# Optimization experiments

Measured on AMD Instinct MI355X. Metric: run time of the kernel, lower is better.

The kernel has to match this reference:

```python
import jax, jax.numpy as jnp
import numpy as np

B, L, E, A, H = 1024, 200, 128, 128, 4

def setup_inputs() -> dict:
    key = jax.random.key(0)
    k1, k2, k3, k4, k5, k6 = jax.random.split(key, 6)
    inp = jax.random.normal(k1, (B, L, E), dtype=jnp.float32)
    mask = jax.random.randint(k2, (B, L), 0, 2).astype(bool)
    # guarantee at least one valid position per row (realistic: histories are non-empty)
    mask = mask.at[:, 0].set(True)
    pos_enc = jax.random.normal(k3, (1, L, E), dtype=jnp.float32)
    W1 = jax.random.normal(k4, (E, A), dtype=jnp.float32) / np.sqrt(E)
    W2 = jax.random.normal(k5, (A, H), dtype=jnp.float32) / np.sqrt(A)
    W_out = jax.random.normal(k6, (H * E, E), dtype=jnp.float32) / np.sqrt(H * E)
    return {"input": inp, "mask": mask, "pos_enc": pos_enc, "W1": W1, "W2": W2, "W_out": W_out}

def reference(input, mask, pos_enc, W1, W2, W_out):
    fm = mask.astype(input.dtype)[..., None]          # [B, L, 1]
    x = input * fm                                     # zero out padded positions
    xp = x + pos_enc                                   # broadcast [1, L, E]
    hidden = jnp.tanh(xp @ W1)                         # [B, L, A]
    att = hidden @ W2                                  # [B, L, H]
    att = jnp.swapaxes(att, 1, 2)                      # [B, H, L]
    neg = jnp.asarray(-(2.0 ** 32) + 1.0, dtype=att.dtype)
    att = jnp.where(mask[:, None, :], att, neg)
    att = jax.nn.softmax(att, axis=-1)                 # [B, H, L]
    pooled = jnp.einsum('bhl,ble->bhe', att, x)        # [B, H, E]
    flat = pooled.reshape(pooled.shape[0], -1)         # [B, H*E]
    return flat @ W_out                                # [B, E]
```

## Files before the change

kernel.cpp:

```cpp
#include <hip/hip_runtime.h>
#include <cfloat>

#define Bn 1024
#define Ln 200
#define En 128
#define An 128
#define Hn 4

#define WS_POSW1   0
#define WS_W1FRAG  106496
#define WS_ATTPOOL 139264
#define SLOT       1664
#define WS_WOUTT   1843200
#define WS_NEEDED  1974272

using f32x4  = __attribute__((ext_vector_type(4))) float;
using bf16x8 = __attribute__((ext_vector_type(8))) short;

__device__ __forceinline__ unsigned short f2bf(float f){
    unsigned u = __builtin_bit_cast(unsigned, f);
    u = (u + 0x7FFFu + ((u >> 16) & 1u)) >> 16;
    return (unsigned short)u;
}
__device__ __forceinline__ float bf2f(unsigned short s){
    unsigned u = ((unsigned)s) << 16;
    return __builtin_bit_cast(float, u);
}
__device__ __forceinline__ float tanh_cheap(float x){
    float e = __expf(2.f * x);
    float r = __builtin_amdgcn_rcpf(e + 1.f);
    return fmaf(-2.f, r, 1.f);
}
__device__ __forceinline__ float tanh_fast(float x){
    x = fminf(fmaxf(x, -12.f), 12.f);
    float e = __expf(2.f * x);
    return 1.f - 2.f / (e + 1.f);
}
__device__ __forceinline__ unsigned cvt_pk_bf16(float lo, float hi){
    unsigned r;
    asm("v_cvt_pk_bf16_f32 %0, %1, %2" : "=v"(r) : "v"(lo), "v"(hi));
    return r;
}
__device__ __forceinline__ int swz(int row, int k){
    return row * 128 + ((((k >> 3) ^ (row & 15)) << 3) | (k & 7));
}

__global__ __launch_bounds__(256) void sap_prep(
    const float* __restrict__ pos, const float* __restrict__ W1,
    const float* __restrict__ Wout, void* __restrict__ ws)
{
    const int t = threadIdx.x, blk = blockIdx.x;
    if (blk < 104){
        float* posW1 = (float*)((char*)ws + WS_POSW1);
        int l = blk * 2 + (t >> 7), a = t & 127;
        float acc = 0.f;
        if (l < Ln){
            #pragma unroll 4
            for (int k = 0; k < 128; ++k)
                acc += pos[l * En + k] * W1[k * An + a];
        }
        posW1[l * An + a] = acc;
    } else if (blk < 106){
        unsigned short* w1f = (unsigned short*)((char*)ws + WS_W1FRAG);
        int s = (blk - 104) * 256 + t;
        int lane = s & 63;
        int A = s >> 6;
        int c = lane & 15, q = lane >> 4;
        #pragma unroll
        for (int ks = 0; ks < 4; ++ks){
            unsigned short v[8];
            #pragma unroll
            for (int j = 0; j < 8; ++j)
                v[j] = f2bf(W1[(ks * 32 + q * 8 + j) * An + A * 16 + c]);
            *(bf16x8*)&w1f[(s * 4 + ks) * 8] = *(bf16x8*)v;
        }
    } else {
        unsigned short* wt = (unsigned short*)((char*)ws + WS_WOUTT);
        int flat = ((blk - 106) * 256 + t) * 4;
        int e = flat >> 9, k = flat & 511;
        unsigned short v[4];
        #pragma unroll
        for (int i = 0; i < 4; ++i)
            v[i] = f2bf(Wout[(size_t)(k + i) * En + e]);
        *(uint2*)&wt[flat] = *(uint2*)v;
    }
}

__global__ __launch_bounds__(512, 4) void sap_att7(
    const float* __restrict__ inp, const void* __restrict__ maskp,
    const float* __restrict__ W2, void* __restrict__ ws)
{
    __shared__ unsigned short s_x[64 * 128];
    __shared__ float s_part[8][4][64];
    __shared__ float s_att4[208 * 4];
    __shared__ float s_scr[16][512];
    __shared__ float s_mask[256];

    const int t = threadIdx.x, lane = t & 63, w = t >> 6;
    const int c = lane & 15, q = lane >> 4;
    const int b = blockIdx.x;

    const unsigned short* w1f   = (const unsigned short*)((char*)ws + WS_W1FRAG);
    const float*          posW1 = (const float*)((char*)ws + WS_POSW1);
    unsigned short*       slot  = (unsigned short*)((char*)ws + WS_ATTPOOL + (size_t)b * SLOT);

    bf16x8 af[4];
    #pragma unroll
    for (int ks = 0; ks < 4; ++ks)
        af[ks] = *(const bf16x8*)&w1f[((w * 64 + lane) * 4 + ks) * 8];
    float4 w2a[4];
    #pragma unroll
    for (int v = 0; v < 4; ++v)
        w2a[v] = *(const float4*)&W2[(w * 16 + q * 4 + v) * Hn];

    {
        unsigned word = ((const unsigned*)maskp)[lane];
        unsigned long long bi  = __ballot(word > 1u);
        unsigned long long bfm = __ballot(word != 0u && word != 0x3F800000u);
        int flag = (bi == 0ull) ? 0 : ((bfm == 0ull) ? 2 : 1);
        if (t < 256){
            float m = 0.f;
            if (t < Ln){
                int mv;
                if (flag == 0)      mv = ((const int*)maskp)[b * Ln + t] != 0;
                else if (flag == 1) mv = ((const unsigned char*)maskp)[b * Ln + t] != 0;
                else                mv = ((const float*)maskp)[b * Ln + t] != 0.f;
                m = mv ? 1.f : 0.f;
            }
            s_mask[t] = m;
        }
    }

    for (int cch = 0; cch < 4; ++cch){
        const int NT = (cch < 3) ? 4 : 1;

        {
            const float4* in4 = (const float4*)(inp + (size_t)b * (Ln * En) + cch * 64 * En);
            #define PUTV(vi, idx) { int ll = (idx) >> 5, kk = ((idx) & 31) * 4;            \
                uint2 val = make_uint2(cvt_pk_bf16(vi.x, vi.y), cvt_pk_bf16(vi.z, vi.w));  \
                *(uint2*)&s_x[swz(ll, kk)] = val; }
            if (cch < 3){
                float4 u0 = in4[t], u1 = in4[t + 512], u2 = in4[t + 1024], u3 = in4[t + 1536];
                PUTV(u0, t) PUTV(u1, t + 512) PUTV(u2, t + 1024) PUTV(u3, t + 1536)
            } else {
                uint2 val = make_uint2(0u, 0u);
                if (t < 256){
                    float4 u0 = in4[t];
                    val = make_uint2(cvt_pk_bf16(u0.x, u0.y), cvt_pk_bf16(u0.z, u0.w));
                }
                int ll = t >> 5, kk = (t & 31) * 4;
                *(uint2*)&s_x[swz(ll, kk)] = val;
            }
            #undef PUTV
        }
        __syncthreads();

        for (int lt = 0; lt < NT; ++lt){
            int brow = lt * 16 + c;
            bf16x8 bfr[4];
            #pragma unroll
            for (int ks = 0; ks < 4; ++ks){
                int g = (ks * 4 + q) ^ c;
                bfr[ks] = *(bf16x8*)&s_x[brow * 128 + (g << 3)];
            }
            f32x4 acc = *(const f32x4*)&posW1[(size_t)(cch * 64 + brow) * An + w * 16 + q * 4];
            #pragma unroll
            for (int ks = 0; ks < 4; ++ks)
                acc = __builtin_amdgcn_mfma_f32_16x16x32_bf16(af[ks], bfr[ks], acc, 0, 0, 0);
            float contrib[4] = {0.f, 0.f, 0.f, 0.f};
            #pragma unroll
            for (int v = 0; v < 4; ++v){
                float hv = tanh_cheap(acc[v]);
                contrib[0] += hv * w2a[v].x;
                contrib[1] += hv * w2a[v].y;
                contrib[2] += hv * w2a[v].z;
                contrib[3] += hv * w2a[v].w;
            }
            #pragma unroll
            for (int h = 0; h < 4; ++h){
                contrib[h] += __shfl_xor(contrib[h], 16, 64);
                contrib[h] += __shfl_xor(contrib[h], 32, 64);
            }
            s_part[w][q][lt * 16 + c] = contrib[q];
        }
        __syncthreads();

        if (t < 256){
            int h = t >> 6, l = t & 63, gl = cch * 64 + l;
            if (gl < Ln){
                float a = 0.f;
                #pragma unroll
                for (int w2 = 0; w2 < 8; ++w2) a += s_part[w2][h][l];
                s_att4[gl * 4 + h] = (s_mask[gl] > 0.5f) ? a : -1.0e30f;
            }
        }
    }
    __syncthreads();

    if (t < 256){
        const int h = t >> 6, sl = t & 63;
        float v[4]; float mx = -FLT_MAX;
        #pragma unroll
        for (int i = 0; i < 4; ++i){
            int l = sl + i * 64;
            v[i] = (l < Ln) ? s_att4[l * 4 + h] : -3.0e38f;
            mx = fmaxf(mx, v[i]);
        }
        for (int s = 32; s; s >>= 1) mx = fmaxf(mx, __shfl_xor(mx, s, 64));
        float e[4]; float sum = 0.f;
        #pragma unroll
        for (int i = 0; i < 4; ++i){
            int l = sl + i * 64;
            e[i] = (l < Ln) ? __expf(v[i] - mx) : 0.f;
            sum += e[i];
        }
        for (int s = 32; s; s >>= 1) sum += __shfl_xor(sum, s, 64);
        float inv = 1.f / sum;
        #pragma unroll
        for (int i = 0; i < 4; ++i){
            int l = sl + i * 64;
            if (l < Ln) s_att4[l * 4 + h] = e[i] * inv;
        }
    }
    __syncthreads();

    {
        const int eg = t & 31, r = t >> 5;
        const float* xin = inp + (size_t)b * (Ln * En);
        f32x4 a0 = {0.f,0.f,0.f,0.f}, a1 = a0, a2 = a0, a3 = a0;
        for (int i = 0; i < 13; ++i){
            int l = i * 16 + r;
            if (l < Ln){
                f32x4 xv = *(const f32x4*)&xin[l * En + eg * 4];
                f32x4 w4 = *(const f32x4*)&s_att4[l * 4];
                a0 += xv * w4[0];
                a1 += xv * w4[1];
                a2 += xv * w4[2];
                a3 += xv * w4[3];
            }
        }
        *(f32x4*)&s_scr[r][0 * 128 + eg * 4] = a0;
        *(f32x4*)&s_scr[r][1 * 128 + eg * 4] = a1;
        *(f32x4*)&s_scr[r][2 * 128 + eg * 4] = a2;
        *(f32x4*)&s_scr[r][3 * 128 + eg * 4] = a3;
    }
    __syncthreads();

    {
        float sum = 0.f;
        #pragma unroll
        for (int r2 = 0; r2 < 16; ++r2) sum += s_scr[r2][t];
        slot[t] = f2bf(sum);
    }
}

__global__ __launch_bounds__(256) void sap_out(
    const void* __restrict__ ws, float* __restrict__ out)
{
    const unsigned short* wt = (const unsigned short*)((const char*)ws + WS_WOUTT);
    const int t = threadIdx.x, lane = t & 63, w = t >> 6;
    const int c = lane & 15, q = lane >> 4;
    const int b0 = blockIdx.x * 16;
    const int e0 = (blockIdx.y * 4 + w) * 16;

    const unsigned short* pslot =
        (const unsigned short*)((const char*)ws + WS_ATTPOOL + (size_t)(b0 + c) * SLOT);

    f32x4 acc = {0.f, 0.f, 0.f, 0.f};
    #pragma unroll 4
    for (int ks = 0; ks < 16; ++ks){
        bf16x8 afr = *(const bf16x8*)&pslot[ks * 32 + q * 8];
        bf16x8 bfr = *(const bf16x8*)&wt[(e0 + c) * 512 + ks * 32 + q * 8];
        acc = __builtin_amdgcn_mfma_f32_16x16x32_bf16(afr, bfr, acc, 0, 0, 0);
    }
    #pragma unroll
    for (int v = 0; v < 4; ++v)
        out[(size_t)(b0 + q * 4 + v) * En + e0 + c] = acc[v];
}

__global__ __launch_bounds__(512, 4) void sap_fused_v2(
    const float* __restrict__ inp, const void* __restrict__ maskp,
    const float* __restrict__ pos, const float* __restrict__ W1,
    const float* __restrict__ W2, const float* __restrict__ Wout,
    float* __restrict__ out)
{
#define LP 208
    __shared__ unsigned short s_xp [LP * 128];
    __shared__ float s_att [4 * LP];
    __shared__ float s_mask[LP];
    __shared__ float s_pool[512];
    __shared__ float s_red [512];
    __shared__ int   s_flag;

    const int t = threadIdx.x;
    const int b = blockIdx.x;
    const int lane = t & 63, w = t >> 6;
    const int c = lane & 15, q = lane >> 4;

    if (t == 0){
        const unsigned* mw = (const unsigned*)maskp;
        int fi = 1, ff = 1;
        for (int i = 0; i < 64; ++i){
            unsigned word = mw[i];
            if (word > 1u) fi = 0;
            if (word != 0u && word != 0x3F800000u) ff = 0;
        }
        s_flag = fi ? 0 : (ff ? 2 : 1);
    }
    bf16x8 af[4];
    {
        const int arow = w * 16 + c;
        #pragma unroll
        for (int ks = 0; ks < 4; ++ks)
            #pragma unroll
            for (int j = 0; j < 8; ++j)
                af[ks][j] = (short)f2bf(W1[(ks * 32 + q * 8 + j) * An + arow]);
    }
    float w2a[4][4];
    #pragma unroll
    for (int v = 0; v < 4; ++v){
        float4 wv = *(const float4*)&W2[(w * 16 + q * 4 + v) * Hn];
        w2a[v][0] = wv.x; w2a[v][1] = wv.y; w2a[v][2] = wv.z; w2a[v][3] = wv.w;
    }
    __syncthreads();
    const int flag = s_flag;
    for (int l = t; l < LP; l += 512){
        float m = 0.f;
        if (l < Ln){
            int mv;
            if (flag == 0)      mv = ((const int*)maskp)[b * Ln + l] != 0;
            else if (flag == 1) mv = ((const unsigned char*)maskp)[b * Ln + l] != 0;
            else                mv = ((const float*)maskp)[b * Ln + l] != 0.f;
            m = mv ? 1.f : 0.f;
        }
        s_mask[l] = m;
    }
    for (int i = t; i < 4 * LP; i += 512) s_att[i] = 0.f;
    __syncthreads();
    {
        const float4* in4 = (const float4*)(inp + (size_t)b * (Ln * En));
        const float4* p4  = (const float4*)pos;
        #pragma unroll
        for (int it = 0; it < 13; ++it){
            int idx = it * 512 + t;
            int l = idx >> 5;
            int k = (idx & 31) * 4;
            uint2 val;
            if (idx < 6400){
                float m = s_mask[l];
                float4 a = in4[idx];
                float4 p = p4[idx];
                val = make_uint2((unsigned)f2bf(a.x*m+p.x) | ((unsigned)f2bf(a.y*m+p.y) << 16),
                                 (unsigned)f2bf(a.z*m+p.z) | ((unsigned)f2bf(a.w*m+p.w) << 16));
            } else val = make_uint2(0u, 0u);
            *(uint2*)&s_xp[swz(l, k)] = val;
        }
    }
    __syncthreads();
    for (int lt = 0; lt < 13; ++lt){
        int brow = lt * 16 + c;
        bf16x8 bfr[4];
        #pragma unroll
        for (int ks = 0; ks < 4; ++ks){
            int g = (ks * 4 + q) ^ c;
            bfr[ks] = *(bf16x8*)&s_xp[brow * 128 + (g << 3)];
        }
        f32x4 acc = {0.f, 0.f, 0.f, 0.f};
        #pragma unroll
        for (int ks = 0; ks < 4; ++ks)
            acc = __builtin_amdgcn_mfma_f32_16x16x32_bf16(af[ks], bfr[ks], acc, 0, 0, 0);
        float hv[4];
        #pragma unroll
        for (int v = 0; v < 4; ++v) hv[v] = tanh_fast(acc[v]);
        #pragma unroll
        for (int h = 0; h < 4; ++h){
            float contrib = hv[0]*w2a[0][h] + hv[1]*w2a[1][h] + hv[2]*w2a[2][h] + hv[3]*w2a[3][h];
            contrib += __shfl_xor(contrib, 16, 64);
            contrib += __shfl_xor(contrib, 32, 64);
            if (lane < 16) atomicAdd(&s_att[h * LP + lt * 16 + lane], contrib);
        }
    }
    __syncthreads();
    if (t < 256){
        const int sl = t & 63, h = t >> 6;
        float v[4]; bool ok[4]; float mx = -FLT_MAX;
        #pragma unroll
        for (int i = 0; i < 4; ++i){
            int l = sl + i * 64;
            ok[i] = (l < Ln) && (s_mask[l] > 0.5f);
            v[i]  = ok[i] ? s_att[h * LP + l] : -FLT_MAX;
            mx = fmaxf(mx, v[i]);
        }
        for (int s = 32; s; s >>= 1) mx = fmaxf(mx, __shfl_xor(mx, s, 64));
        float e[4]; float sum = 0.f;
        #pragma unroll
        for (int i = 0; i < 4; ++i){ e[i] = ok[i] ? __expf(v[i]-mx) : 0.f; sum += e[i]; }
        for (int s = 32; s; s >>= 1) sum += __shfl_xor(sum, s, 64);
        float inv = 1.f / sum;
        #pragma unroll
        for (int i = 0; i < 4; ++i){ int l = sl + i*64; if (l < LP) s_att[h*LP+l] = e[i]*inv; }
    }
    __syncthreads();
    {
        int h = t >> 7, e = t & 127;
        float acc = 0.f;
        #pragma unroll 4
        for (int l = 0; l < Ln; ++l){
            float xv = bf2f(s_xp[swz(l, e)]) - pos[l * En + e];
            acc += s_att[h * LP + l] * xv;
        }
        s_pool[h * En + e] = acc;
    }
    __syncthreads();
    {
        int qt = t >> 7, e = t & 127;
        float acc = 0.f;
        const float* wo = Wout + (size_t)(qt * 128) * En + e;
        #pragma unroll 4
        for (int i = 0; i < 128; ++i)
            acc += s_pool[qt * 128 + i] * wo[(size_t)i * En];
        s_red[t] = acc;
    }
    __syncthreads();
    if (t < 128)
        out[(size_t)b * En + t] = s_red[t] + s_red[t + 128] + s_red[t + 256] + s_red[t + 384];
#undef LP
}

extern "C" void kernel_launch(void* const* d_in, const int* in_sizes, int n_in,
                              void* d_out, int out_size, void* d_ws, size_t ws_size,
                              hipStream_t stream)
{
    const float* inp  = (const float*)d_in[0];
    const void*  mask = d_in[1];
    const float* pos  = (const float*)d_in[2];
    const float* W1   = (const float*)d_in[3];
    const float* W2   = (const float*)d_in[4];
    const float* Wout = (const float*)d_in[5];
    float* out = (float*)d_out;

    if (ws_size >= WS_NEEDED){
        sap_prep<<<170, 256, 0, stream>>>(pos, W1, Wout, d_ws);
        sap_att7<<<Bn, 512, 0, stream>>>(inp, mask, W2, d_ws);
        sap_out<<<dim3(64, 2), 256, 0, stream>>>(d_ws, out);
    } else {
        sap_fused_v2<<<Bn, 512, 0, stream>>>(inp, mask, pos, W1, W2, Wout, out);
    }
}
```

Measured before the change: 64.60 us.

## Keep all input chunks in LDS as bf16 and pool from shared memory

```diff
diff --git a/kernel.cpp b/kernel.cpp
--- a/kernel.cpp
+++ b/kernel.cpp
@@ -86,14 +86,13 @@
     }
 }
 
-__global__ __launch_bounds__(512, 4) void sap_att7(
+__global__ __launch_bounds__(512, 4) void sap_att9(
     const float* __restrict__ inp, const void* __restrict__ maskp,
     const float* __restrict__ W2, void* __restrict__ ws)
 {
-    __shared__ unsigned short s_x[64 * 128];
+    __shared__ unsigned short s_x4[4][64 * 128];
     __shared__ float s_part[8][4][64];
     __shared__ float s_att4[208 * 4];
-    __shared__ float s_scr[16][512];
     __shared__ float s_mask[256];
 
     const int t = threadIdx.x, lane = t & 63, w = t >> 6;
@@ -133,6 +132,7 @@
 
     for (int cch = 0; cch < 4; ++cch){
         const int NT = (cch < 3) ? 4 : 1;
+        unsigned short* s_x = &s_x4[cch][0];
 
         {
             const float4* in4 = (const float4*)(inp + (size_t)b * (Ln * En) + cch * 64 * En);
@@ -225,32 +225,14 @@
     __syncthreads();
 
     {
-        const int eg = t & 31, r = t >> 5;
-        const float* xin = inp + (size_t)b * (Ln * En);
-        f32x4 a0 = {0.f,0.f,0.f,0.f}, a1 = a0, a2 = a0, a3 = a0;
-        for (int i = 0; i < 13; ++i){
-            int l = i * 16 + r;
-            if (l < Ln){
-                f32x4 xv = *(const f32x4*)&xin[l * En + eg * 4];
-                f32x4 w4 = *(const f32x4*)&s_att4[l * 4];
-                a0 += xv * w4[0];
-                a1 += xv * w4[1];
-                a2 += xv * w4[2];
-                a3 += xv * w4[3];
-            }
-        }
-        *(f32x4*)&s_scr[r][0 * 128 + eg * 4] = a0;
-        *(f32x4*)&s_scr[r][1 * 128 + eg * 4] = a1;
-        *(f32x4*)&s_scr[r][2 * 128 + eg * 4] = a2;
-        *(f32x4*)&s_scr[r][3 * 128 + eg * 4] = a3;
-    }
-    __syncthreads();
-
-    {
-        float sum = 0.f;
-        #pragma unroll
-        for (int r2 = 0; r2 < 16; ++r2) sum += s_scr[r2][t];
-        slot[t] = f2bf(sum);
+        const int h = t >> 7, e = t & 127;
+        float acc = 0.f;
+        #pragma unroll 8
+        for (int l = 0; l < Ln; ++l){
+            float xv = bf2f(s_x4[l >> 6][swz(l & 63, e)]);
+            acc = fmaf(s_att4[l * 4 + h], xv, acc);
+        }
+        slot[h * En + e] = f2bf(acc);
     }
 }
 
@@ -441,7 +423,7 @@
 
     if (ws_size >= WS_NEEDED){
         sap_prep<<<170, 256, 0, stream>>>(pos, W1, Wout, d_ws);
-        sap_att7<<<Bn, 512, 0, stream>>>(inp, mask, W2, d_ws);
+        sap_att9<<<Bn, 512, 0, stream>>>(inp, mask, W2, d_ws);
         sap_out<<<dim3(64, 2), 256, 0, stream>>>(d_ws, out);
     } else {
         sap_fused_v2<<<Bn, 512, 0, stream>>>(inp, mask, pos, W1, W2, Wout, out);
```

New measurement: 67.69 us. 4.8% more time.

## Double block size to process two sequence chunks concurrently in attention kernel

Applied to the files above, without the earlier changes.

```diff
diff --git a/kernel.cpp b/kernel.cpp
--- a/kernel.cpp
+++ b/kernel.cpp
@@ -86,18 +86,19 @@
     }
 }
 
-__global__ __launch_bounds__(512, 4) void sap_att7(
+__global__ __launch_bounds__(1024, 4) void sap_att13(
     const float* __restrict__ inp, const void* __restrict__ maskp,
     const float* __restrict__ W2, void* __restrict__ ws)
 {
-    __shared__ unsigned short s_x[64 * 128];
-    __shared__ float s_part[8][4][64];
+    __shared__ __align__(16) char smem_u[49152];
     __shared__ float s_att4[208 * 4];
-    __shared__ float s_scr[16][512];
     __shared__ float s_mask[256];
+
+    float (*s_scr)[512] = (float (*)[512])smem_u;
 
     const int t = threadIdx.x, lane = t & 63, w = t >> 6;
     const int c = lane & 15, q = lane >> 4;
+    const int wsub = w & 7, wg = w >> 3;
     const int b = blockIdx.x;
 
     const unsigned short* w1f   = (const unsigned short*)((char*)ws + WS_W1FRAG);
@@ -107,11 +108,11 @@
     bf16x8 af[4];
     #pragma unroll
     for (int ks = 0; ks < 4; ++ks)
-        af[ks] = *(const bf16x8*)&w1f[((w * 64 + lane) * 4 + ks) * 8];
+        af[ks] = *(const bf16x8*)&w1f[((wsub * 64 + lane) * 4 + ks) * 8];
     float4 w2a[4];
     #pragma unroll
     for (int v = 0; v < 4; ++v)
-        w2a[v] = *(const float4*)&W2[(w * 16 + q * 4 + v) * Hn];
+        w2a[v] = *(const float4*)&W2[(wsub * 16 + q * 4 + v) * Hn];
 
     {
         unsigned word = ((const unsigned*)maskp)[lane];
@@ -131,70 +132,84 @@
         }
     }
 
-    for (int cch = 0; cch < 4; ++cch){
-        const int NT = (cch < 3) ? 4 : 1;
-
+    #define SXBUF(g)  ((unsigned short*)(smem_u + (g) * 16384))
+    #define SPART(g)  ((float*)(smem_u + 32768 + (g) * 8192))
+    #define PUTV(sx, vi, idx) { int ll = (idx) >> 5, kk = ((idx) & 31) * 4;            \
+        uint2 val = make_uint2(cvt_pk_bf16(vi.x, vi.y), cvt_pk_bf16(vi.z, vi.w));      \
+        *(uint2*)&(sx)[swz(ll, kk)] = val; }
+
+    for (int it = 0; it < 2; ++it){
         {
-            const float4* in4 = (const float4*)(inp + (size_t)b * (Ln * En) + cch * 64 * En);
-            #define PUTV(vi, idx) { int ll = (idx) >> 5, kk = ((idx) & 31) * 4;            \
-                uint2 val = make_uint2(cvt_pk_bf16(vi.x, vi.y), cvt_pk_bf16(vi.z, vi.w));  \
-                *(uint2*)&s_x[swz(ll, kk)] = val; }
-            if (cch < 3){
-                float4 u0 = in4[t], u1 = in4[t + 512], u2 = in4[t + 1024], u3 = in4[t + 1536];
-                PUTV(u0, t) PUTV(u1, t + 512) PUTV(u2, t + 1024) PUTV(u3, t + 1536)
+            const int sg = t >> 9, tl = t & 511;
+            const int scch = it * 2 + sg;
+            unsigned short* sx = SXBUF(sg);
+            const float4* in4 = (const float4*)(inp + (size_t)b * (Ln * En) + scch * 64 * En);
+            if (scch < 3){
+                float4 u0 = in4[tl], u1 = in4[tl + 512], u2 = in4[tl + 1024], u3 = in4[tl + 1536];
+                PUTV(sx, u0, tl) PUTV(sx, u1, tl + 512) PUTV(sx, u2, tl + 1024) PUTV(sx, u3, tl + 1536)
             } else {
                 uint2 val = make_uint2(0u, 0u);
-                if (t < 256){
-                    float4 u0 = in4[t];
+                if (tl < 256){
+                    float4 u0 = in4[tl];
                     val = make_uint2(cvt_pk_bf16(u0.x, u0.y), cvt_pk_bf16(u0.z, u0.w));
                 }
-                int ll = t >> 5, kk = (t & 31) * 4;
-                *(uint2*)&s_x[swz(ll, kk)] = val;
+                int ll = tl >> 5, kk = (tl & 31) * 4;
+                *(uint2*)&sx[swz(ll, kk)] = val;
             }
-            #undef PUTV
         }
         __syncthreads();
 
-        for (int lt = 0; lt < NT; ++lt){
-            int brow = lt * 16 + c;
-            bf16x8 bfr[4];
-            #pragma unroll
-            for (int ks = 0; ks < 4; ++ks){
-                int g = (ks * 4 + q) ^ c;
-                bfr[ks] = *(bf16x8*)&s_x[brow * 128 + (g << 3)];
+        {
+            unsigned short* s_x = SXBUF(wg);
+            float* spart = SPART(wg);
+            const int cch = it * 2 + wg;
+            const int NT = (cch < 3) ? 4 : 1;
+            for (int lt = 0; lt < NT; ++lt){
+                int brow = lt * 16 + c;
+                bf16x8 bfr[4];
+                #pragma unroll
+                for (int ks = 0; ks < 4; ++ks){
+                    int g = (ks * 4 + q) ^ c;
+                    bfr[ks] = *(bf16x8*)&s_x[brow * 128 + (g << 3)];
+                }
+                f32x4 acc = *(const f32x4*)&posW1[(size_t)(cch * 64 + brow) * An + wsub * 16 + q * 4];
+                #pragma unroll
+                for (int ks = 0; ks < 4; ++ks)
+                    acc = __builtin_amdgcn_mfma_f32_16x16x32_bf16(af[ks], bfr[ks], acc, 0, 0, 0);
+                float contrib[4] = {0.f, 0.f, 0.f, 0.f};
+                #pragma unroll
+                for (int v = 0; v < 4; ++v){
+                    float hv = tanh_cheap(acc[v]);
+                    contrib[0] += hv * w2a[v].x;
+                    contrib[1] += hv * w2a[v].y;
+                    contrib[2] += hv * w2a[v].z;
+                    contrib[3] += hv * w2a[v].w;
+                }
+                #pragma unroll
+                for (int h = 0; h < 4; ++h){
+                    contrib[h] += __shfl_xor(contrib[h], 16, 64);
+                    contrib[h] += __shfl_xor(contrib[h], 32, 64);
+                }
+                spart[(wsub * 4 + q) * 64 + lt * 16 + c] = contrib[q];
             }
-            f32x4 acc = *(const f32x4*)&posW1[(size_t)(cch * 64 + brow) * An + w * 16 + q * 4];
-            #pragma unroll
-            for (int ks = 0; ks < 4; ++ks)
-                acc = __builtin_amdgcn_mfma_f32_16x16x32_bf16(af[ks], bfr[ks], acc, 0, 0, 0);
-            float contrib[4] = {0.f, 0.f, 0.f, 0.f};
-            #pragma unroll
-            for (int v = 0; v < 4; ++v){
-                float hv = tanh_cheap(acc[v]);
-                contrib[0] += hv * w2a[v].x;
-                contrib[1] += hv * w2a[v].y;
-                contrib[2] += hv * w2a[v].z;
-                contrib[3] += hv * w2a[v].w;
-            }
-            #pragma unroll
-            for (int h = 0; h < 4; ++h){
-                contrib[h] += __shfl_xor(contrib[h], 16, 64);
-                contrib[h] += __shfl_xor(contrib[h], 32, 64);
-            }
-            s_part[w][q][lt * 16 + c] = contrib[q];
         }
         __syncthreads();
 
-        if (t < 256){
-            int h = t >> 6, l = t & 63, gl = cch * 64 + l;
+        if (t < 512){
+            int g2 = t >> 8, h = (t >> 6) & 3, l = t & 63;
+            int gl = (it * 2 + g2) * 64 + l;
             if (gl < Ln){
+                const float* sp = SPART(g2);
                 float a = 0.f;
                 #pragma unroll
-                for (int w2 = 0; w2 < 8; ++w2) a += s_part[w2][h][l];
+                for (int w2 = 0; w2 < 8; ++w2) a += sp[(w2 * 4 + h) * 64 + l];
                 s_att4[gl * 4 + h] = (s_mask[gl] > 0.5f) ? a : -1.0e30f;
             }
         }
     }
+    #undef PUTV
+    #undef SPART
+    #undef SXBUF
     __syncthreads();
 
     if (t < 256){
@@ -224,7 +239,7 @@
     }
     __syncthreads();
 
-    {
+    if (t < 512){
         const int eg = t & 31, r = t >> 5;
         const float* xin = inp + (size_t)b * (Ln * En);
         f32x4 a0 = {0.f,0.f,0.f,0.f}, a1 = a0, a2 = a0, a3 = a0;
@@ -246,7 +261,7 @@
     }
     __syncthreads();
 
-    {
+    if (t < 512){
         float sum = 0.f;
         #pragma unroll
         for (int r2 = 0; r2 < 16; ++r2) sum += s_scr[r2][t];
@@ -441,7 +456,7 @@
 
     if (ws_size >= WS_NEEDED){
         sap_prep<<<170, 256, 0, stream>>>(pos, W1, Wout, d_ws);
-        sap_att7<<<Bn, 512, 0, stream>>>(inp, mask, W2, d_ws);
+        sap_att13<<<Bn, 1024, 0, stream>>>(inp, mask, W2, d_ws);
         sap_out<<<dim3(64, 2), 256, 0, stream>>>(d_ws, out);
     } else {
         sap_fused_v2<<<Bn, 512, 0, stream>>>(inp, mask, pos, W1, W2, Wout, out);
```

After: 70.06 us. 1.08x slower.
